# Performance work log

Hardware: AMD Instinct MI355X
Metric: run time of the kernel (lower is better)

## Reference

```python
import jax, jax.numpy as jnp
import numpy as np

D_MODEL = 2048
NUM_HEADS = 16
D_K = D_MODEL // NUM_HEADS
MAX_SEQ_LEN = 2048


def setup_inputs() -> dict:
    key = jax.random.key(0)
    ks = jax.random.split(key, 9)
    s = 1.0 / np.sqrt(D_MODEL)
    x = jax.random.normal(ks[0], (4, 2048, D_MODEL), dtype=jnp.float32)
    Wq = jax.random.normal(ks[1], (D_MODEL, D_MODEL), dtype=jnp.float32) * s
    bq = jnp.zeros((D_MODEL,), dtype=jnp.float32)
    Wk = jax.random.normal(ks[2], (D_MODEL, D_MODEL), dtype=jnp.float32) * s
    bk = jnp.zeros((D_MODEL,), dtype=jnp.float32)
    Wv = jax.random.normal(ks[3], (D_MODEL, D_MODEL), dtype=jnp.float32) * s
    bv = jnp.zeros((D_MODEL,), dtype=jnp.float32)
    Wo = jax.random.normal(ks[4], (D_MODEL, D_MODEL), dtype=jnp.float32) * s
    bo = jnp.zeros((D_MODEL,), dtype=jnp.float32)
    return {"x": x, "Wq": Wq, "bq": bq, "Wk": Wk, "bk": bk,
            "Wv": Wv, "bv": bv, "Wo": Wo, "bo": bo}


def _rope_tables(seq_len, d_k, dtype):
    # GPT-NeoX style rotate-half RoPE tables: [seq_len, d_k]
    inv_freq = 1.0 / (10000.0 ** (np.arange(0, d_k, 2, dtype=np.float32) / d_k))
    pos = np.arange(seq_len, dtype=np.float32)
    freqs = np.outer(pos, inv_freq)              # [S, d_k/2]
    emb = np.concatenate([freqs, freqs], axis=-1)  # [S, d_k]
    return jnp.asarray(np.cos(emb), dtype=dtype), jnp.asarray(np.sin(emb), dtype=dtype)


def _apply_rope(x, cos, sin):
    # x: [B, H, S, d_k]; rotate-half
    x1, x2 = jnp.split(x, 2, axis=-1)
    rotated = jnp.concatenate([-x2, x1], axis=-1)
    return x * cos + rotated * sin


def reference(x, Wq, bq, Wk, bk, Wv, bv, Wo, bo):
    B, S, _ = x.shape
    cos, sin = _rope_tables(S, D_K, x.dtype)  # [S, d_k]

    def split_heads(t):  # [B,S,D] -> [B,H,S,d_k]
        return t.reshape(B, S, NUM_HEADS, D_K).transpose(0, 2, 1, 3)

    q = split_heads(x @ Wq.T + bq)
    k = split_heads(x @ Wk.T + bk)
    v = split_heads(x @ Wv.T + bv)

    q = _apply_rope(q, cos, sin)
    k = _apply_rope(k, cos, sin)

    scale = 1.0 / jnp.sqrt(jnp.asarray(D_K, dtype=x.dtype))
    scores = jnp.einsum("bhqd,bhkd->bhqk", q, k) * scale
    attn = jax.nn.softmax(scores, axis=-1)
    out = jnp.einsum("bhqk,bhkd->bhqd", attn, v)  # [B,H,S,d_k]
    out = out.transpose(0, 2, 1, 3).reshape(B, S, D_MODEL)
    return out @ Wo.T + bo
```

## Files before the change

### kernel.cpp

```cpp
#include <hip/hip_runtime.h>
#include <hip/hip_bf16.h>
#include <math.h>

typedef __bf16 bf16;
typedef __bf16 bf16x2 __attribute__((ext_vector_type(2)));
typedef __bf16 bf16x4 __attribute__((ext_vector_type(4)));
typedef __bf16 bf16x8 __attribute__((ext_vector_type(8)));
typedef float f32x4 __attribute__((ext_vector_type(4)));

#define D_MODEL 2048
#define SEQ 2048
#define BATCH 4
#define NH 16
#define DK 128

typedef const __attribute__((address_space(1))) void* as1_ptr;
typedef __attribute__((address_space(3))) void* as3_ptr;

__device__ __forceinline__ void gld_lds16(const bf16* g, bf16* l) {
  __builtin_amdgcn_global_load_lds((as1_ptr)g, (as3_ptr)l, 16, 0, 0);
}

__global__ void cvt_kernel(const float* __restrict__ in, bf16* __restrict__ out, int n8) {
  int i = blockIdx.x * 256 + threadIdx.x;
  if (i >= n8) return;
  long base = (long)i * 8;
  const float4* p = (const float4*)(in + base);
  float4 a = p[0], b = p[1];
  bf16x8 v;
  v[0] = (bf16)a.x; v[1] = (bf16)a.y; v[2] = (bf16)a.z; v[3] = (bf16)a.w;
  v[4] = (bf16)b.x; v[5] = (bf16)b.y; v[6] = (bf16)b.z; v[7] = (bf16)b.w;
  *(bf16x8*)(out + base) = v;
}

__global__ void cvt4_kernel(const float* a, const float* b, const float* c, const float* d,
                            bf16* oa, bf16* ob, bf16* oc, bf16* od) {
  const float* in; bf16* out;
  switch (blockIdx.y) {
    case 0: in = a; out = oa; break;
    case 1: in = b; out = ob; break;
    case 2: in = c; out = oc; break;
    default: in = d; out = od; break;
  }
  int i = blockIdx.x * 256 + threadIdx.x;
  long base = (long)i * 8;
  const float4* p = (const float4*)(in + base);
  float4 x = p[0], y = p[1];
  bf16x8 v;
  v[0] = (bf16)x.x; v[1] = (bf16)x.y; v[2] = (bf16)x.z; v[3] = (bf16)x.w;
  v[4] = (bf16)y.x; v[5] = (bf16)y.y; v[6] = (bf16)y.z; v[7] = (bf16)y.w;
  *(bf16x8*)(out + base) = v;
}

template<int OUT_F32, int BIAS_ROW>
__global__ __launch_bounds__(256, 2)
void gemm_nt(const bf16* __restrict__ A, const bf16* __restrict__ B,
             const float* __restrict__ bias, void* __restrict__ Cout, int K, int ldc)
{
  __shared__ alignas(16) bf16 As[128 * 32];
  __shared__ alignas(16) bf16 Bs[128 * 32];
  const int tid  = threadIdx.x;
  const int wave = tid >> 6, lane = tid & 63;
  const int quad = lane >> 4, l16 = lane & 15;
  const int n0 = blockIdx.x * 128, m0 = blockIdx.y * 128;
  const int wm = (wave >> 1) * 64, wn = (wave & 1) * 64;

  const int srow = tid >> 2, scol = (tid & 3) * 8;
  const bf16* Ag1 = A + (long)(m0 + srow) * K + scol;
  const bf16* Ag2 = Ag1 + (long)64 * K;
  const bf16* Bg1 = B + (long)(n0 + srow) * K + scol;
  const bf16* Bg2 = Bg1 + (long)64 * K;
  bf16* Asw = As + wave * 512;
  bf16* Bsw = Bs + wave * 512;

  f32x4 acc[4][4] = {};
  for (int k0 = 0; k0 < K; k0 += 32) {
    __syncthreads();
    gld_lds16(Ag1 + k0, Asw);
    gld_lds16(Ag2 + k0, Asw + 2048);
    gld_lds16(Bg1 + k0, Bsw);
    gld_lds16(Bg2 + k0, Bsw + 2048);
    __syncthreads();
    bf16x8 Af[4], Bf[4];
    for (int mi = 0; mi < 4; mi++)
      Af[mi] = *(const bf16x8*)(&As[(wm + mi * 16 + l16) * 32 + quad * 8]);
    for (int ni = 0; ni < 4; ni++)
      Bf[ni] = *(const bf16x8*)(&Bs[(wn + ni * 16 + l16) * 32 + quad * 8]);
    for (int mi = 0; mi < 4; mi++)
      for (int ni = 0; ni < 4; ni++)
        acc[mi][ni] = __builtin_amdgcn_mfma_f32_16x16x32_bf16(Af[mi], Bf[ni], acc[mi][ni], 0, 0, 0);
  }

  float bv[4];
  if (!BIAS_ROW)
    for (int ni = 0; ni < 4; ni++) bv[ni] = bias[n0 + wn + ni * 16 + l16];
  for (int mi = 0; mi < 4; mi++)
    for (int r = 0; r < 4; r++) {
      long row = m0 + wm + mi * 16 + quad * 4 + r;
      float bm = BIAS_ROW ? bias[row] : 0.0f;
      for (int ni = 0; ni < 4; ni++) {
        float v = acc[mi][ni][r] + (BIAS_ROW ? bm : bv[ni]);
        long idx = row * (long)ldc + n0 + wn + ni * 16 + l16;
        if (OUT_F32) ((float*)Cout)[idx] = v;
        else         ((bf16*)Cout)[idx] = (bf16)v;
      }
    }
}

__global__ void ropetab_kernel(float* __restrict__ ctab) {
  int idx = blockIdx.x * 256 + threadIdx.x;
  int j = idx & 63, p = idx >> 6;
  float f = exp2f(-(float)j * 0.20762050593046f);
  float th = (float)p * f;
  ctab[idx * 2]     = cosf(th);
  ctab[idx * 2 + 1] = sinf(th);
}

__global__ void rope_kernel(bf16* __restrict__ Q, bf16* __restrict__ K,
                            const float* __restrict__ ctab) {
  long idx = (long)blockIdx.x * 256 + threadIdx.x;
  bf16* P = blockIdx.y ? K : Q;
  int i2 = (int)(idx & 31);
  int h  = (int)((idx >> 5) & 15);
  long row = idx >> 9;
  int pos = (int)(row & (SEQ - 1));
  float4 cs = *(const float4*)(ctab + ((long)pos * 64 + 2 * i2) * 2);
  long base = row * D_MODEL + h * DK + 2 * i2;
  bf16x2 x1 = *(bf16x2*)(P + base);
  bf16x2 x2 = *(bf16x2*)(P + base + 64);
  bf16x2 y1, y2;
  y1[0] = (bf16)((float)x1[0] * cs.x - (float)x2[0] * cs.y);
  y2[0] = (bf16)((float)x2[0] * cs.x + (float)x1[0] * cs.y);
  y1[1] = (bf16)((float)x1[1] * cs.z - (float)x2[1] * cs.w);
  y2[1] = (bf16)((float)x2[1] * cs.z + (float)x1[1] * cs.w);
  *(bf16x2*)(P + base)      = y1;
  *(bf16x2*)(P + base + 64) = y2;
}

__global__ __launch_bounds__(256, 2)
void attn_kernel(const bf16* __restrict__ Q, const bf16* __restrict__ K,
                 const bf16* __restrict__ Vt, bf16* __restrict__ O)
{
  __shared__ alignas(16) bf16 Ks[64 * 128];
  __shared__ alignas(16) bf16 Vts[128 * 64];
  __shared__ alignas(16) bf16 Ps[128 * 72];
  const int tid  = threadIdx.x;
  const int wave = tid >> 6, lane = tid & 63;
  const int quad = lane >> 4, l16 = lane & 15;
  const int qt = blockIdx.x, bh = blockIdx.y;
  const int b = bh >> 4, h = bh & 15;
  const long qrow0 = (long)b * SEQ + qt * 128;
  const bf16* Qb = Q + qrow0 * D_MODEL + h * DK;
  const bf16* Kb = K + (long)b * SEQ * D_MODEL + h * DK;
  const bf16* Vb = Vt + (long)(h * DK) * (BATCH * SEQ) + b * SEQ;

  bf16x8 Qf[2][4];
  for (int ni = 0; ni < 2; ni++)
    for (int ks = 0; ks < 4; ks++)
      Qf[ni][ks] = *(const bf16x8*)(Qb + (long)(wave * 32 + ni * 16 + l16) * D_MODEL + ks * 32 + quad * 8);

  const bf16* Ksrc[4]; const bf16* Vsrc[4];
  for (int i = 0; i < 4; i++) {
    int g = wave * 4 + i;
    int rk = 4 * g + (lane >> 4);
    int ck = l16 ^ (rk & 7);
    Ksrc[i] = Kb + (long)rk * D_MODEL + ck * 8;
    int rv = 8 * g + (lane >> 3);
    int cv = (lane & 7) ^ (rv & 7);
    Vsrc[i] = Vb + (long)rv * (BATCH * SEQ) + cv * 8;
  }

  f32x4 Oacc[8][2] = {};
  float lsum[2] = {0.0f, 0.0f};
  const float kSc = 0.088388347648318447f * 1.4426950408889634f;
  const int swz = l16 & 7;

  for (int kt = 0; kt < SEQ; kt += 64) {
    __syncthreads();
    for (int i = 0; i < 4; i++)
      gld_lds16(Ksrc[i] + (long)kt * D_MODEL, Ks + (wave * 4 + i) * 512);
    for (int i = 0; i < 4; i++)
      gld_lds16(Vsrc[i] + kt, Vts + (wave * 4 + i) * 512);
    __syncthreads();

    f32x4 Sc[4][2] = {};
    for (int ks = 0; ks < 4; ks++) {
      bf16x8 Kf[4];
      for (int si = 0; si < 4; si++) {
        int c = (ks * 4 + quad) ^ swz;
        Kf[si] = *(const bf16x8*)(&Ks[(si * 16 + l16) * 128 + c * 8]);
      }
      for (int si = 0; si < 4; si++)
        for (int ni = 0; ni < 2; ni++)
          Sc[si][ni] = __builtin_amdgcn_mfma_f32_16x16x32_bf16(Kf[si], Qf[ni][ks], Sc[si][ni], 0, 0, 0);
    }

    for (int si = 0; si < 4; si++)
      for (int ni = 0; ni < 2; ni++) {
        bf16x4 pk;
        for (int r = 0; r < 4; r++) {
          float p = exp2f(Sc[si][ni][r] * kSc);
          lsum[ni] += p;
          pk[r] = (bf16)p;
        }
        *(bf16x4*)(&Ps[(wave * 32 + ni * 16 + l16) * 72 + si * 16 + quad * 4]) = pk;
      }

    for (int k2 = 0; k2 < 2; k2++) {
      bf16x8 Pf[2];
      for (int ni = 0; ni < 2; ni++)
        Pf[ni] = *(const bf16x8*)(&Ps[(wave * 32 + ni * 16 + l16) * 72 + k2 * 32 + quad * 8]);
      for (int mi = 0; mi < 8; mi++) {
        int c = (k2 * 4 + quad) ^ swz;
        bf16x8 Vf = *(const bf16x8*)(&Vts[(mi * 16 + l16) * 64 + c * 8]);
        for (int ni = 0; ni < 2; ni++)
          Oacc[mi][ni] = __builtin_amdgcn_mfma_f32_16x16x32_bf16(Vf, Pf[ni], Oacc[mi][ni], 0, 0, 0);
      }
    }
  }

  for (int ni = 0; ni < 2; ni++) {
    lsum[ni] += __shfl_xor(lsum[ni], 16);
    lsum[ni] += __shfl_xor(lsum[ni], 32);
  }

  for (int ni = 0; ni < 2; ni++) {
    float rinv = 1.0f / lsum[ni];
    long rowbase = (qrow0 + wave * 32 + ni * 16 + l16) * (long)D_MODEL + h * DK + quad * 4;
    for (int mi = 0; mi < 8; mi++) {
      bf16x4 o;
      for (int r = 0; r < 4; r++) o[r] = (bf16)(Oacc[mi][ni][r] * rinv);
      *(bf16x4*)(O + rowbase + mi * 16) = o;
    }
  }
}

extern "C" void kernel_launch(void* const* d_in, const int* in_sizes, int n_in,
                              void* d_out, int out_size, void* d_ws, size_t ws_size,
                              hipStream_t stream) {
  const float* x  = (const float*)d_in[0];
  const float* Wq = (const float*)d_in[1];
  const float* bq = (const float*)d_in[2];
  const float* Wk = (const float*)d_in[3];
  const float* bk = (const float*)d_in[4];
  const float* Wv = (const float*)d_in[5];
  const float* bv = (const float*)d_in[6];
  const float* Wo = (const float*)d_in[7];
  const float* bo = (const float*)d_in[8];
  float* out = (float*)d_out;

  bf16* ws = (bf16*)d_ws;
  bf16* xb  = ws;
  bf16* Wqb = ws + 16777216;
  bf16* Wkb = ws + 20971520;
  bf16* Wvb = ws + 25165824;
  bf16* Wob = ws + 29360128;
  bf16* Qp  = ws + 33554432;
  bf16* Kp  = ws + 50331648;
  bf16* VtF = ws + 67108864;
  float* ctab = (float*)ws;
  bf16* O   = xb;

  cvt_kernel<<<8192, 256, 0, stream>>>(x, xb, 2097152);
  cvt4_kernel<<<dim3(2048, 4), 256, 0, stream>>>(Wq, Wk, Wv, Wo, Wqb, Wkb, Wvb, Wob);

  dim3 gg(16, 64);
  gemm_nt<0, 0><<<gg, 256, 0, stream>>>(xb, Wqb, bq, Qp, 2048, 2048);
  gemm_nt<0, 0><<<gg, 256, 0, stream>>>(xb, Wkb, bk, Kp, 2048, 2048);
  gemm_nt<0, 1><<<dim3(64, 16), 256, 0, stream>>>(Wvb, xb, bv, VtF, 2048, 8192);

  ropetab_kernel<<<512, 256, 0, stream>>>(ctab);
  rope_kernel<<<dim3(16384, 2), 256, 0, stream>>>(Qp, Kp, ctab);

  attn_kernel<<<dim3(16, 64), 256, 0, stream>>>(Qp, Kp, VtF, O);

  gemm_nt<1, 0><<<gg, 256, 0, stream>>>(O, Wob, bo, out, 2048, 2048);
}
```

Measured before the change: 699.1 us.

## Double attention query tile per block and fold softmax scale into RoPE

Each attention block now handles 256 query rows instead of 128, so every wave computes 64 rows and each K/V tile loaded into shared memory is reused across twice as many queries. The loop is restructured per key subtile to keep fewer score registers live. The softmax scale and log2(e) factor are folded into Q during the RoPE pass, which removes a multiply per score, and the row sums are accumulated as vectors. In exchange the kernel holds twice the accumulator registers and twice the P buffer in shared memory, and launches only 512 blocks, which risks lower occupancy or spilling.

After: 777.0 us. +11.1%, slower.

```diff
diff --git a/kernel.cpp b/kernel.cpp
--- a/kernel.cpp
+++ b/kernel.cpp
@@ -120,6 +120,8 @@
                             const float* __restrict__ ctab) {
   long idx = (long)blockIdx.x * 256 + threadIdx.x;
   bf16* P = blockIdx.y ? K : Q;
+  const float sc = blockIdx.y ? 1.0f
+                 : 0.0883883476483184f * 1.4426950408889634f;
   int i2 = (int)(idx & 31);
   int h  = (int)((idx >> 5) & 15);
   long row = idx >> 9;
@@ -129,10 +131,10 @@
   bf16x2 x1 = *(bf16x2*)(P + base);
   bf16x2 x2 = *(bf16x2*)(P + base + 64);
   bf16x2 y1, y2;
-  y1[0] = (bf16)((float)x1[0] * cs.x - (float)x2[0] * cs.y);
-  y2[0] = (bf16)((float)x2[0] * cs.x + (float)x1[0] * cs.y);
-  y1[1] = (bf16)((float)x1[1] * cs.z - (float)x2[1] * cs.w);
-  y2[1] = (bf16)((float)x2[1] * cs.z + (float)x1[1] * cs.w);
+  y1[0] = (bf16)(((float)x1[0] * cs.x - (float)x2[0] * cs.y) * sc);
+  y2[0] = (bf16)(((float)x2[0] * cs.x + (float)x1[0] * cs.y) * sc);
+  y1[1] = (bf16)(((float)x1[1] * cs.z - (float)x2[1] * cs.w) * sc);
+  y2[1] = (bf16)(((float)x2[1] * cs.z + (float)x1[1] * cs.w) * sc);
   *(bf16x2*)(P + base)      = y1;
   *(bf16x2*)(P + base + 64) = y2;
 }
@@ -143,21 +145,21 @@
 {
   __shared__ alignas(16) bf16 Ks[64 * 128];
   __shared__ alignas(16) bf16 Vts[128 * 64];
-  __shared__ alignas(16) bf16 Ps[128 * 72];
+  __shared__ alignas(16) bf16 Ps[256 * 72];
   const int tid  = threadIdx.x;
   const int wave = tid >> 6, lane = tid & 63;
   const int quad = lane >> 4, l16 = lane & 15;
   const int qt = blockIdx.x, bh = blockIdx.y;
   const int b = bh >> 4, h = bh & 15;
-  const long qrow0 = (long)b * SEQ + qt * 128;
+  const long qrow0 = (long)b * SEQ + qt * 256;
   const bf16* Qb = Q + qrow0 * D_MODEL + h * DK;
   const bf16* Kb = K + (long)b * SEQ * D_MODEL + h * DK;
   const bf16* Vb = Vt + (long)(h * DK) * (BATCH * SEQ) + b * SEQ;
 
-  bf16x8 Qf[2][4];
-  for (int ni = 0; ni < 2; ni++)
+  bf16x8 Qf[4][4];
+  for (int ni = 0; ni < 4; ni++)
     for (int ks = 0; ks < 4; ks++)
-      Qf[ni][ks] = *(const bf16x8*)(Qb + (long)(wave * 32 + ni * 16 + l16) * D_MODEL + ks * 32 + quad * 8);
+      Qf[ni][ks] = *(const bf16x8*)(Qb + (long)(wave * 64 + ni * 16 + l16) * D_MODEL + ks * 32 + quad * 8);
 
   const bf16* Ksrc[4]; const bf16* Vsrc[4];
   for (int i = 0; i < 4; i++) {
@@ -170,10 +172,10 @@
     Vsrc[i] = Vb + (long)rv * (BATCH * SEQ) + cv * 8;
   }
 
-  f32x4 Oacc[8][2] = {};
-  float lsum[2] = {0.0f, 0.0f};
-  const float kSc = 0.088388347648318447f * 1.4426950408889634f;
+  f32x4 Oacc[8][4] = {};
+  f32x4 ls4[4] = {};
   const int swz = l16 & 7;
+  const int prow = (wave * 64 + l16) * 72;
 
   for (int kt = 0; kt < SEQ; kt += 64) {
     __syncthreads();
@@ -183,50 +185,50 @@
       gld_lds16(Vsrc[i] + kt, Vts + (wave * 4 + i) * 512);
     __syncthreads();
 
-    f32x4 Sc[4][2] = {};
-    for (int ks = 0; ks < 4; ks++) {
-      bf16x8 Kf[4];
-      for (int si = 0; si < 4; si++) {
+    for (int si = 0; si < 4; si++) {
+      f32x4 Sc[4] = {};
+      for (int ks = 0; ks < 4; ks++) {
         int c = (ks * 4 + quad) ^ swz;
-        Kf[si] = *(const bf16x8*)(&Ks[(si * 16 + l16) * 128 + c * 8]);
-      }
-      for (int si = 0; si < 4; si++)
-        for (int ni = 0; ni < 2; ni++)
-          Sc[si][ni] = __builtin_amdgcn_mfma_f32_16x16x32_bf16(Kf[si], Qf[ni][ks], Sc[si][ni], 0, 0, 0);
-    }
-
-    for (int si = 0; si < 4; si++)
-      for (int ni = 0; ni < 2; ni++) {
+        bf16x8 Kf = *(const bf16x8*)(&Ks[(si * 16 + l16) * 128 + c * 8]);
+        for (int ni = 0; ni < 4; ni++)
+          Sc[ni] = __builtin_amdgcn_mfma_f32_16x16x32_bf16(Kf, Qf[ni][ks], Sc[ni], 0, 0, 0);
+      }
+      for (int ni = 0; ni < 4; ni++) {
+        f32x4 p4;
+        p4[0] = exp2f(Sc[ni][0]);
+        p4[1] = exp2f(Sc[ni][1]);
+        p4[2] = exp2f(Sc[ni][2]);
+        p4[3] = exp2f(Sc[ni][3]);
+        ls4[ni] += p4;
         bf16x4 pk;
-        for (int r = 0; r < 4; r++) {
-          float p = exp2f(Sc[si][ni][r] * kSc);
-          lsum[ni] += p;
-          pk[r] = (bf16)p;
-        }
-        *(bf16x4*)(&Ps[(wave * 32 + ni * 16 + l16) * 72 + si * 16 + quad * 4]) = pk;
-      }
+        pk[0] = (bf16)p4[0]; pk[1] = (bf16)p4[1]; pk[2] = (bf16)p4[2]; pk[3] = (bf16)p4[3];
+        *(bf16x4*)(&Ps[prow + ni * 16 * 72 + si * 16 + quad * 4]) = pk;
+      }
+    }
 
     for (int k2 = 0; k2 < 2; k2++) {
-      bf16x8 Pf[2];
-      for (int ni = 0; ni < 2; ni++)
-        Pf[ni] = *(const bf16x8*)(&Ps[(wave * 32 + ni * 16 + l16) * 72 + k2 * 32 + quad * 8]);
+      bf16x8 Pf[4];
+      for (int ni = 0; ni < 4; ni++)
+        Pf[ni] = *(const bf16x8*)(&Ps[prow + ni * 16 * 72 + k2 * 32 + quad * 8]);
       for (int mi = 0; mi < 8; mi++) {
         int c = (k2 * 4 + quad) ^ swz;
         bf16x8 Vf = *(const bf16x8*)(&Vts[(mi * 16 + l16) * 64 + c * 8]);
-        for (int ni = 0; ni < 2; ni++)
+        for (int ni = 0; ni < 4; ni++)
           Oacc[mi][ni] = __builtin_amdgcn_mfma_f32_16x16x32_bf16(Vf, Pf[ni], Oacc[mi][ni], 0, 0, 0);
       }
     }
   }
 
-  for (int ni = 0; ni < 2; ni++) {
+  float lsum[4];
+  for (int ni = 0; ni < 4; ni++) {
+    lsum[ni] = ls4[ni][0] + ls4[ni][1] + ls4[ni][2] + ls4[ni][3];
     lsum[ni] += __shfl_xor(lsum[ni], 16);
     lsum[ni] += __shfl_xor(lsum[ni], 32);
   }
 
-  for (int ni = 0; ni < 2; ni++) {
+  for (int ni = 0; ni < 4; ni++) {
     float rinv = 1.0f / lsum[ni];
-    long rowbase = (qrow0 + wave * 32 + ni * 16 + l16) * (long)D_MODEL + h * DK + quad * 4;
+    long rowbase = (qrow0 + wave * 64 + ni * 16 + l16) * (long)D_MODEL + h * DK + quad * 4;
     for (int mi = 0; mi < 8; mi++) {
       bf16x4 o;
       for (int r = 0; r < 4; r++) o[r] = (bf16)(Oacc[mi][ni][r] * rinv);
@@ -272,7 +274,7 @@
   ropetab_kernel<<<512, 256, 0, stream>>>(ctab);
   rope_kernel<<<dim3(16384, 2), 256, 0, stream>>>(Qp, Kp, ctab);
 
-  attn_kernel<<<dim3(16, 64), 256, 0, stream>>>(Qp, Kp, VtF, O);
+  attn_kernel<<<dim3(8, 64), 256, 0, stream>>>(Qp, Kp, VtF, O);
 
   gemm_nt<1, 0><<<gg, 256, 0, stream>>>(O, Wob, bo, out, 2048, 2048);
 }
```
